# Performance work log

Hardware: AMD Instinct MI355X
Metric: run time of the kernel (lower is better)

The kernel has to match this reference:

```python
import jax, jax.numpy as jnp
import numpy as np
from jax import lax

C = 64
EPS = 1e-6

def ln2d(x, w, b):
    # channel-wise LN over HxW per (n, c)
    mean = x.mean(axis=(2, 3), keepdims=True)
    var = ((x - mean) ** 2).mean(axis=(2, 3), keepdims=True)
    return (x - mean) / jnp.sqrt(var + EPS) * w + b

def pw(x, w, b):
    # 1x1 conv: w [O, I], b [O]
    return jnp.einsum('nihw,oi->nohw', x, w) + b[None, :, None, None]

def dwconv3(x, w, b):
    # depthwise 3x3, w [2C, 1, 3, 3]
    y = lax.conv_general_dilated(x, w, window_strides=(1, 1), padding='SAME',
                                 feature_group_count=x.shape[1],
                                 dimension_numbers=('NCHW', 'OIHW', 'NCHW'))
    return y + b[None, :, None, None]

def simple_gate(x):
    x1, x2 = jnp.split(x, 2, axis=1)
    return x1 * x2

def setup_inputs() -> dict:
    key = jax.random.key(0)
    ks = jax.random.split(key, 16)
    s = 0.05
    return {
        'x': jax.random.normal(ks[0], (8, C, 256, 256), jnp.float32),
        'ln1_w': jnp.ones((1, C, 1, 1), jnp.float32),
        'ln1_b': jnp.zeros((1, C, 1, 1), jnp.float32),
        'pw1_w': jax.random.normal(ks[1], (2 * C, C), jnp.float32) * s,
        'pw1_b': jnp.zeros((2 * C,), jnp.float32),
        'dw_w': jax.random.normal(ks[2], (2 * C, 1, 3, 3), jnp.float32) * s,
        'dw_b': jnp.zeros((2 * C,), jnp.float32),
        'sca_w': jax.random.normal(ks[3], (C, C), jnp.float32) * s,
        'sca_b': jnp.zeros((C,), jnp.float32),
        'pw2_w': jax.random.normal(ks[4], (C, C), jnp.float32) * s,
        'pw2_b': jnp.zeros((C,), jnp.float32),
        'ln2_w': jnp.ones((1, C, 1, 1), jnp.float32),
        'ln2_b': jnp.zeros((1, C, 1, 1), jnp.float32),
        'pw3_w': jax.random.normal(ks[5], (2 * C, C), jnp.float32) * s,
        'pw3_b': jnp.zeros((2 * C,), jnp.float32),
        'pw4_w': jax.random.normal(ks[6], (C, C), jnp.float32) * s,
        'pw4_b': jnp.zeros((C,), jnp.float32),
        'beta1': jax.random.normal(ks[7], (1, C, 1, 1), jnp.float32) * 0.1,
        'beta2': jax.random.normal(ks[8], (1, C, 1, 1), jnp.float32) * 0.1,
    }

def reference(x, ln1_w, ln1_b, pw1_w, pw1_b, dw_w, dw_b, sca_w, sca_b,
              pw2_w, pw2_b, ln2_w, ln2_b, pw3_w, pw3_b, pw4_w, pw4_b,
              beta1, beta2):
    y = ln2d(x, ln1_w, ln1_b)
    y = pw(y, pw1_w, pw1_b)
    y = dwconv3(y, dw_w, dw_b)
    y = simple_gate(y)
    # SCA: global avg pool -> 1x1 conv -> sigmoid scale
    s = y.mean(axis=(2, 3), keepdims=True)          # [N, C, 1, 1]
    w = jax.nn.sigmoid(pw(s, sca_w, sca_b))
    y = y * w
    y = pw(y, pw2_w, pw2_b)
    x = x + beta1 * y
    y2 = ln2d(x, ln2_w, ln2_b)
    y2 = pw(y2, pw3_w, pw3_b)
    y2 = simple_gate(y2)
    y2 = pw(y2, pw4_w, pw4_b)
    return x + beta2 * y2
```

## Files before the change

### kernel.cpp

```cpp
#include <hip/hip_runtime.h>
#include <hip/hip_bf16.h>

#define NB 8
#define HWP 65536

typedef __attribute__((ext_vector_type(8))) short short8;
typedef __attribute__((ext_vector_type(4))) float f32x4;

__device__ __forceinline__ short f2bf(float f) {
  union { float f; unsigned u; } v; v.f = f;
  return (short)((v.u + 0x7FFF + ((v.u >> 16) & 1)) >> 16);
}
__device__ __forceinline__ float bf2f(unsigned short u) {
  union { unsigned u; float f; } v; v.u = ((unsigned)u) << 16; return v.f;
}

__global__ __launch_bounds__(512) void ln_stats_kernel(
    const float* __restrict__ x, const float* __restrict__ lw,
    const float* __restrict__ lb, float* __restrict__ a, float* __restrict__ b) {
  int plane = blockIdx.x;
  int c = plane & 63;
  const float4* p4 = (const float4*)(x + (size_t)plane * HWP);
  float s = 0.f, s2 = 0.f;
  for (int i = threadIdx.x; i < HWP / 4; i += 512) {
    float4 v = p4[i];
    s  += v.x + v.y + v.z + v.w;
    s2 += v.x * v.x + v.y * v.y + v.z * v.z + v.w * v.w;
  }
  for (int off = 32; off; off >>= 1) {
    s  += __shfl_down(s, off);
    s2 += __shfl_down(s2, off);
  }
  __shared__ float ls[8], ls2[8];
  int wid = threadIdx.x >> 6, lid = threadIdx.x & 63;
  if (lid == 0) { ls[wid] = s; ls2[wid] = s2; }
  __syncthreads();
  if (threadIdx.x == 0) {
    float S = 0.f, S2 = 0.f;
    for (int k = 0; k < 8; k++) { S += ls[k]; S2 += ls2[k]; }
    float mean = S * (1.f / (float)HWP);
    float var  = S2 * (1.f / (float)HWP) - mean * mean;
    float rstd = rsqrtf(var + 1e-6f);
    float av = rstd * lw[c];
    a[plane] = av;
    b[plane] = lb[c] - mean * av;
  }
}

__global__ void fold_kernel(const float* __restrict__ w, const float* __restrict__ pb,
                            const float* __restrict__ a, const float* __restrict__ b,
                            unsigned short* __restrict__ wf16, float* __restrict__ cf, int O) {
  int idx = blockIdx.x * blockDim.x + threadIdx.x;
  if (idx >= NB * O) return;
  int n = idx / O, o = idx - n * O;
  int MT = O >> 4;
  const float* an = a + n * 64;
  const float* bn = b + n * 64;
  const float* wo = w + o * 64;
  int mt = o >> 4, cl = o & 15;
  float cc = pb[o];
  for (int i = 0; i < 64; i++) {
    float wv = wo[i];
    float wf = wv * an[i];
    cc += wv * bn[i];
    int ks = i >> 5, quad = (i >> 3) & 3, j = i & 7;
    wf16[((((size_t)(n * MT + mt) * 2 + ks) * 16 + cl) * 4 + quad) * 8 + j] =
        (unsigned short)f2bf(wf);
  }
  cf[idx] = cc;
}

__global__ __launch_bounds__(256, 2) void gemm_pw1_kernel(
    const float* __restrict__ x, const unsigned short* __restrict__ wf16,
    const float* __restrict__ cf, unsigned short* __restrict__ z) {
  int n = blockIdx.y;
  int lane = threadIdx.x & 63, wid = threadIdx.x >> 6;
  int col = lane & 15, quad = lane >> 4;
  const short8* wv8 = (const short8*)wf16 + (size_t)n * 1024;
  short8 a[8][2];
  #pragma unroll
  for (int mt = 0; mt < 8; mt++)
    #pragma unroll
    for (int ks = 0; ks < 2; ks++)
      a[mt][ks] = wv8[((mt * 2 + ks) * 16 + col) * 4 + quad];
  f32x4 cb[8];
  #pragma unroll
  for (int mt = 0; mt < 8; mt++)
    cb[mt] = *(const f32x4*)(cf + n * 128 + mt * 16 + quad * 4);
  const float* xn = x + (size_t)n * 64 * HWP;
  unsigned short* zn = z + (size_t)n * 128 * HWP;
  int pxbase = blockIdx.x * 128 + wid * 16 + col;

  auto load_b = [&](int p, short8* bf) {
    #pragma unroll
    for (int ks = 0; ks < 2; ks++) {
      short8 v;
      #pragma unroll
      for (int j = 0; j < 8; j++)
        v[j] = f2bf(xn[(size_t)(ks * 32 + quad * 8 + j) * HWP + p]);
      bf[ks] = v;
    }
  };

  short8 bb[2][2];
  load_b(pxbase, bb[0]);
  #pragma unroll
  for (int tile = 0; tile < 2; tile++) {
    int cur = tile & 1, nxt = cur ^ 1;
    int p = pxbase + tile * 64;
    if (tile < 1) load_b(p + 64, bb[nxt]);
    f32x4 acc[8];
    #pragma unroll
    for (int mt = 0; mt < 8; mt++) {
      acc[mt] = cb[mt];
      acc[mt] = __builtin_amdgcn_mfma_f32_16x16x32_bf16(a[mt][0], bb[cur][0], acc[mt], 0, 0, 0);
      acc[mt] = __builtin_amdgcn_mfma_f32_16x16x32_bf16(a[mt][1], bb[cur][1], acc[mt], 0, 0, 0);
    }
    #pragma unroll
    for (int mt = 0; mt < 8; mt++)
      #pragma unroll
      for (int r = 0; r < 4; r++)
        zn[(size_t)(mt * 16 + quad * 4 + r) * HWP + p] =
            (unsigned short)f2bf(acc[mt][r]);
  }
}

__global__ __launch_bounds__(256) void dwgate_kernel(
    const unsigned short* __restrict__ z, const float* __restrict__ dww,
    const float* __restrict__ dwb, unsigned short* __restrict__ t,
    float* __restrict__ pooled4) {
  int blk = blockIdx.x;
  int plane = blk >> 2, qtr = blk & 3;
  int n = plane >> 6, c = plane & 63;
  int lane = threadIdx.x & 63, wv = threadIdx.x >> 6;
  const unsigned short* z0 = z + ((size_t)n * 128 + c) * HWP;
  const unsigned short* z1 = z0 + (size_t)64 * HWP;
  unsigned short* tp = t + (size_t)plane * HWP;
  float w0[9], w1[9];
  #pragma unroll
  for (int k = 0; k < 9; k++) { w0[k] = dww[c * 9 + k]; w1[k] = dww[(c + 64) * 9 + k]; }
  float bias0 = dwb[c], bias1 = dwb[c + 64];
  int r0 = qtr * 64 + wv * 16;
  int colb = lane * 4;

  float fa[3][4], la[3], ra[3];
  float fb[3][4], lb_[3], rb[3];

  auto loadrow = [&](const unsigned short* base, int h, float* f, float& l, float& r) {
    if ((unsigned)h < 256u) {
      ushort4 u = *(const ushort4*)(base + h * 256 + colb);
      f[0] = bf2f(u.x); f[1] = bf2f(u.y); f[2] = bf2f(u.z); f[3] = bf2f(u.w);
    } else {
      f[0] = f[1] = f[2] = f[3] = 0.f;
    }
    float ll = __shfl_up(f[3], 1);
    float rr = __shfl_down(f[0], 1);
    l = (lane == 0) ? 0.f : ll;
    r = (lane == 63) ? 0.f : rr;
  };

  loadrow(z0, r0 - 1, fa[0], la[0], ra[0]);
  loadrow(z1, r0 - 1, fb[0], lb_[0], rb[0]);
  loadrow(z0, r0,     fa[1], la[1], ra[1]);
  loadrow(z1, r0,     fb[1], lb_[1], rb[1]);

  float lsum = 0.f;
  #pragma unroll 2
  for (int h = r0; h < r0 + 16; h++) {
    loadrow(z0, h + 1, fa[2], la[2], ra[2]);
    loadrow(z1, h + 1, fb[2], lb_[2], rb[2]);
    float o0[4] = {bias0, bias0, bias0, bias0};
    float o1[4] = {bias1, bias1, bias1, bias1};
    #pragma unroll
    for (int rr_ = 0; rr_ < 3; rr_++) {
      float wl0 = w0[rr_ * 3], wc0 = w0[rr_ * 3 + 1], wr0 = w0[rr_ * 3 + 2];
      float wl1 = w1[rr_ * 3], wc1 = w1[rr_ * 3 + 1], wr1 = w1[rr_ * 3 + 2];
      const float* f0 = fa[rr_]; const float* f1 = fb[rr_];
      float l0 = la[rr_], r0h = ra[rr_], l1 = lb_[rr_], r1h = rb[rr_];
      o0[0] += wl0 * l0    + wc0 * f0[0] + wr0 * f0[1];
      o0[1] += wl0 * f0[0] + wc0 * f0[1] + wr0 * f0[2];
      o0[2] += wl0 * f0[1] + wc0 * f0[2] + wr0 * f0[3];
      o0[3] += wl0 * f0[2] + wc0 * f0[3] + wr0 * r0h;
      o1[0] += wl1 * l1    + wc1 * f1[0] + wr1 * f1[1];
      o1[1] += wl1 * f1[0] + wc1 * f1[1] + wr1 * f1[2];
      o1[2] += wl1 * f1[1] + wc1 * f1[2] + wr1 * f1[3];
      o1[3] += wl1 * f1[2] + wc1 * f1[3] + wr1 * r1h;
    }
    float g0 = o0[0] * o1[0], g1 = o0[1] * o1[1];
    float g2 = o0[2] * o1[2], g3 = o0[3] * o1[3];
    uint2 pk;
    pk.x = (unsigned)(unsigned short)f2bf(g0) | ((unsigned)(unsigned short)f2bf(g1) << 16);
    pk.y = (unsigned)(unsigned short)f2bf(g2) | ((unsigned)(unsigned short)f2bf(g3) << 16);
    *(uint2*)(tp + (size_t)h * 256 + colb) = pk;
    lsum += (g0 + g1) + (g2 + g3);
    #pragma unroll
    for (int i = 0; i < 4; i++) { fa[0][i] = fa[1][i]; fa[1][i] = fa[2][i];
                                  fb[0][i] = fb[1][i]; fb[1][i] = fb[2][i]; }
    la[0] = la[1]; la[1] = la[2]; ra[0] = ra[1]; ra[1] = ra[2];
    lb_[0] = lb_[1]; lb_[1] = lb_[2]; rb[0] = rb[1]; rb[1] = rb[2];
  }
  for (int off = 32; off; off >>= 1) lsum += __shfl_down(lsum, off);
  __shared__ float ls[4];
  if (lane == 0) ls[wv] = lsum;
  __syncthreads();
  if (threadIdx.x == 0) pooled4[plane * 4 + qtr] = ls[0] + ls[1] + ls[2] + ls[3];
}

__global__ void sca_kernel(const float* __restrict__ pooled4, const float* __restrict__ sw,
                           const float* __restrict__ sb, float* __restrict__ sca) {
  int idx = blockIdx.x * blockDim.x + threadIdx.x;
  if (idx >= 512) return;
  int n = idx >> 6, o = idx & 63;
  float s = sb[o];
  const float* pm = pooled4 + n * 256;
  for (int i = 0; i < 64; i++)
    s += sw[o * 64 + i] * (pm[i * 4] + pm[i * 4 + 1] + pm[i * 4 + 2] + pm[i * 4 + 3]) *
         (1.f / 65536.f);
  sca[idx] = 1.f / (1.f + expf(-s));
}

__global__ void fold_pw2_kernel(const float* __restrict__ w, const float* __restrict__ pb,
                                const float* __restrict__ sca, const float* __restrict__ beta1,
                                unsigned short* __restrict__ wf16, float* __restrict__ cf) {
  int idx = blockIdx.x * blockDim.x + threadIdx.x;
  if (idx >= 512) return;
  int n = idx >> 6, o = idx & 63;
  float bt = beta1[o];
  const float* sn = sca + n * 64;
  int mt = o >> 4, cl = o & 15;
  for (int i = 0; i < 64; i++) {
    float wf = bt * w[o * 64 + i] * sn[i];
    int ks = i >> 5, quad = (i >> 3) & 3, j = i & 7;
    wf16[((((size_t)(n * 4 + mt) * 2 + ks) * 16 + cl) * 4 + quad) * 8 + j] =
        (unsigned short)f2bf(wf);
  }
  cf[idx] = bt * pb[o];
}

__global__ void fold4_kernel(const float* __restrict__ w4, const float* __restrict__ pb4,
                             const float* __restrict__ beta2,
                             unsigned short* __restrict__ wf16, float* __restrict__ cf) {
  int o = threadIdx.x;
  if (o >= 64) return;
  float bt = beta2[o];
  int mt = o >> 4, cl = o & 15;
  for (int i = 0; i < 64; i++) {
    int ks = i >> 5, quad = (i >> 3) & 3, j = i & 7;
    wf16[((((size_t)mt * 2 + ks) * 16 + cl) * 4 + quad) * 8 + j] =
        (unsigned short)f2bf(bt * w4[o * 64 + i]);
  }
  cf[o] = bt * pb4[o];
}

__global__ __launch_bounds__(256, 2) void gemm_pw2_kernel(
    const unsigned short* __restrict__ t, const float* __restrict__ x,
    const unsigned short* __restrict__ wf16, const float* __restrict__ cf,
    float* __restrict__ x1, float* __restrict__ part_sum, float* __restrict__ part_sq) {
  __shared__ float red_s[4][64], red_q[4][64];
  int n = blockIdx.y;
  int lane = threadIdx.x & 63, wid = threadIdx.x >> 6;
  int col = lane & 15, quad = lane >> 4;
  const short8* wv8 = (const short8*)wf16 + (size_t)n * 512;
  short8 a[4][2];
  #pragma unroll
  for (int mt = 0; mt < 4; mt++)
    #pragma unroll
    for (int ks = 0; ks < 2; ks++)
      a[mt][ks] = wv8[((mt * 2 + ks) * 16 + col) * 4 + quad];
  f32x4 cb[4];
  #pragma unroll
  for (int mt = 0; mt < 4; mt++)
    cb[mt] = *(const f32x4*)(cf + n * 64 + mt * 16 + quad * 4);
  const unsigned short* tn = t + (size_t)n * 64 * HWP;
  const float* xn = x + (size_t)n * 64 * HWP;
  float* x1n = x1 + (size_t)n * 64 * HWP;
  int pxbase = blockIdx.x * 128 + wid * 16 + col;

  auto load_t = [&](int p, short8* bf) {
    #pragma unroll
    for (int ks = 0; ks < 2; ks++) {
      short8 v;
      #pragma unroll
      for (int j = 0; j < 8; j++)
        v[j] = (short)tn[(size_t)(ks * 32 + quad * 8 + j) * HWP + p];
      bf[ks] = v;
    }
  };
  auto load_x = [&](int p, float (*xv)[4]) {
    #pragma unroll
    for (int mt = 0; mt < 4; mt++)
      #pragma unroll
      for (int r = 0; r < 4; r++)
        xv[mt][r] = xn[(size_t)(mt * 16 + quad * 4 + r) * HWP + p];
  };

  float sacc[4][4], qacc[4][4];
  #pragma unroll
  for (int mt = 0; mt < 4; mt++)
    #pragma unroll
    for (int r = 0; r < 4; r++) { sacc[mt][r] = 0.f; qacc[mt][r] = 0.f; }

  short8 bb[2][2];
  float xv[2][4][4];
  load_t(pxbase, bb[0]);
  load_x(pxbase, xv[0]);
  #pragma unroll
  for (int tile = 0; tile < 2; tile++) {
    int cur = tile & 1, nxt = cur ^ 1;
    int p = pxbase + tile * 64;
    if (tile < 1) { load_t(p + 64, bb[nxt]); load_x(p + 64, xv[nxt]); }
    f32x4 acc[4];
    #pragma unroll
    for (int mt = 0; mt < 4; mt++) {
      acc[mt] = cb[mt];
      acc[mt] = __builtin_amdgcn_mfma_f32_16x16x32_bf16(a[mt][0], bb[cur][0], acc[mt], 0, 0, 0);
      acc[mt] = __builtin_amdgcn_mfma_f32_16x16x32_bf16(a[mt][1], bb[cur][1], acc[mt], 0, 0, 0);
    }
    #pragma unroll
    for (int mt = 0; mt < 4; mt++)
      #pragma unroll
      for (int r = 0; r < 4; r++) {
        size_t idx = (size_t)(mt * 16 + quad * 4 + r) * HWP + p;
        float v = xv[cur][mt][r] + acc[mt][r];
        x1n[idx] = v;
        sacc[mt][r] += v;
        qacc[mt][r] += v * v;
      }
  }
  #pragma unroll
  for (int mt = 0; mt < 4; mt++)
    #pragma unroll
    for (int r = 0; r < 4; r++) {
      float s = sacc[mt][r], q = qacc[mt][r];
      #pragma unroll
      for (int off = 1; off < 16; off <<= 1) {
        s += __shfl_xor(s, off);
        q += __shfl_xor(q, off);
      }
      if (col == 0) {
        int o = mt * 16 + quad * 4 + r;
        red_s[wid][o] = s; red_q[wid][o] = q;
      }
    }
  __syncthreads();
  if (threadIdx.x < 64) {
    int c = threadIdx.x;
    float s = red_s[0][c] + red_s[1][c] + red_s[2][c] + red_s[3][c];
    float q = red_q[0][c] + red_q[1][c] + red_q[2][c] + red_q[3][c];
    size_t pidx = ((size_t)n * 64 + c) * 512 + blockIdx.x;
    part_sum[pidx] = s;
    part_sq[pidx]  = q;
  }
}

__global__ __launch_bounds__(256) void ln2fold_kernel(
    const float* __restrict__ w, const float* __restrict__ pb,
    const float* __restrict__ ps, const float* __restrict__ pq,
    const float* __restrict__ lw, const float* __restrict__ lb,
    unsigned short* __restrict__ wf16, float* __restrict__ cf) {
  __shared__ float aa[64], bbv[64];
  int n = blockIdx.x;
  if (threadIdx.x < 64) {
    int c = threadIdx.x;
    const float* p1 = ps + ((size_t)n * 64 + c) * 512;
    const float* p2 = pq + ((size_t)n * 64 + c) * 512;
    float S = 0.f, S2 = 0.f;
    for (int k = 0; k < 512; k++) { S += p1[k]; S2 += p2[k]; }
    float mean = S * (1.f / (float)HWP);
    float var  = S2 * (1.f / (float)HWP) - mean * mean;
    float rstd = rsqrtf(var + 1e-6f);
    float av = rstd * lw[c];
    aa[c] = av;
    bbv[c] = lb[c] - mean * av;
  }
  __syncthreads();
  if (threadIdx.x < 128) {
    int o = threadIdx.x;
    const float* wo = w + o * 64;
    int mt = o >> 4, cl = o & 15;
    float cc = pb[o];
    for (int i = 0; i < 64; i++) {
      float wv = wo[i];
      float wf = wv * aa[i];
      cc += wv * bbv[i];
      int ks = i >> 5, quad = (i >> 3) & 3, j = i & 7;
      wf16[((((size_t)(n * 8 + mt) * 2 + ks) * 16 + cl) * 4 + quad) * 8 + j] =
          (unsigned short)f2bf(wf);
    }
    cf[n * 128 + o] = cc;
  }
}

__global__ __launch_bounds__(256, 2) void final_mfma_kernel(
    const float* __restrict__ x1, const unsigned short* __restrict__ w3f16,
    const float* __restrict__ c3f, const unsigned short* __restrict__ w4f16,
    const float* __restrict__ c4f, float* __restrict__ out) {
  __shared__ float s_c3[128];
  __shared__ __align__(16) float s_c4[64];
  int n = blockIdx.y;
  int lane = threadIdx.x & 63, wid = threadIdx.x >> 6;
  int col = lane & 15, quad = lane >> 4;
  if (threadIdx.x < 128) s_c3[threadIdx.x] = c3f[n * 128 + threadIdx.x];
  if (threadIdx.x < 64) s_c4[threadIdx.x] = c4f[threadIdx.x];
  const short8* w3v = (const short8*)w3f16 + (size_t)n * 1024;
  short8 a3[8][2];
  #pragma unroll
  for (int mt = 0; mt < 8; mt++)
    #pragma unroll
    for (int ks = 0; ks < 2; ks++)
      a3[mt][ks] = w3v[((mt * 2 + ks) * 16 + col) * 4 + quad];
  const short8* w4v = (const short8*)w4f16;
  short8 a4[4][2];
  #pragma unroll
  for (int mt = 0; mt < 4; mt++)
    #pragma unroll
    for (int ks = 0; ks < 2; ks++)
      a4[mt][ks] = w4v[((mt * 2 + ks) * 16 + col) * 4 + quad];
  __syncthreads();
  const float* x1n = x1 + (size_t)n * 64 * HWP;
  float* outn = out + (size_t)n * 64 * HWP;
  int pxbase = blockIdx.x * 128 + wid * 16 + col;

  auto load_b1 = [&](int p, short8* bf) {
    #pragma unroll
    for (int ks = 0; ks < 2; ks++) {
      short8 v;
      #pragma unroll
      for (int j = 0; j < 8; j++)
        v[j] = f2bf(x1n[(size_t)(ks * 32 + quad * 8 + j) * HWP + p]);
      bf[ks] = v;
    }
  };

  short8 bb1[2][2];
  load_b1(pxbase, bb1[0]);
  #pragma unroll
  for (int tile = 0; tile < 2; tile++) {
    int cur = tile & 1, nxt = cur ^ 1;
    int p = pxbase + tile * 64;
    if (tile < 1) load_b1(p + 64, bb1[nxt]);
    f32x4 acc[8];
    #pragma unroll
    for (int mt = 0; mt < 8; mt++) {
      acc[mt] = (f32x4){0.f, 0.f, 0.f, 0.f};
      acc[mt] = __builtin_amdgcn_mfma_f32_16x16x32_bf16(a3[mt][0], bb1[cur][0], acc[mt], 0, 0, 0);
      acc[mt] = __builtin_amdgcn_mfma_f32_16x16x32_bf16(a3[mt][1], bb1[cur][1], acc[mt], 0, 0, 0);
    }
    unsigned pd[4][2];
    #pragma unroll
    for (int mt = 0; mt < 4; mt++)
      #pragma unroll
      for (int u = 0; u < 2; u++) {
        int c0 = mt * 16 + quad * 4 + 2 * u;
        float ga = (acc[mt][2 * u]     + s_c3[c0])     * (acc[mt + 4][2 * u]     + s_c3[64 + c0]);
        float gb = (acc[mt][2 * u + 1] + s_c3[c0 + 1]) * (acc[mt + 4][2 * u + 1] + s_c3[64 + c0 + 1]);
        pd[mt][u] = (unsigned)(unsigned short)f2bf(ga) |
                    ((unsigned)(unsigned short)f2bf(gb) << 16);
      }
    short8 b2f[2];
    #pragma unroll
    for (int ks = 0; ks < 2; ks++)
      #pragma unroll
      for (int w = 0; w < 4; w++) {
        int src = ((quad & 1) * 2 + (w >> 1)) * 16 + col;
        unsigned v0 = (unsigned)__shfl((int)pd[ks * 2][w & 1], src, 64);
        unsigned v1 = (unsigned)__shfl((int)pd[ks * 2 + 1][w & 1], src, 64);
        unsigned u = (quad & 2) ? v1 : v0;
        b2f[ks][2 * w]     = (short)(u & 0xFFFFu);
        b2f[ks][2 * w + 1] = (short)(u >> 16);
      }
    f32x4 acc2[4];
    #pragma unroll
    for (int mt = 0; mt < 4; mt++) {
      acc2[mt] = *(const f32x4*)&s_c4[mt * 16 + quad * 4];
      acc2[mt] = __builtin_amdgcn_mfma_f32_16x16x32_bf16(a4[mt][0], b2f[0], acc2[mt], 0, 0, 0);
      acc2[mt] = __builtin_amdgcn_mfma_f32_16x16x32_bf16(a4[mt][1], b2f[1], acc2[mt], 0, 0, 0);
    }
    #pragma unroll
    for (int mt = 0; mt < 4; mt++)
      #pragma unroll
      for (int r = 0; r < 4; r++) {
        size_t idx = (size_t)(mt * 16 + quad * 4 + r) * HWP + p;
        outn[idx] = x1n[idx] + acc2[mt][r];
      }
  }
}

extern "C" void kernel_launch(void* const* d_in, const int* in_sizes, int n_in,
                              void* d_out, int out_size, void* d_ws, size_t ws_size,
                              hipStream_t stream) {
  const float* x    = (const float*)d_in[0];
  const float* ln1w = (const float*)d_in[1];
  const float* ln1b = (const float*)d_in[2];
  const float* pw1w = (const float*)d_in[3];
  const float* pw1b = (const float*)d_in[4];
  const float* dww  = (const float*)d_in[5];
  const float* dwb  = (const float*)d_in[6];
  const float* scaw = (const float*)d_in[7];
  const float* scab = (const float*)d_in[8];
  const float* pw2w = (const float*)d_in[9];
  const float* pw2b = (const float*)d_in[10];
  const float* ln2w = (const float*)d_in[11];
  const float* ln2b = (const float*)d_in[12];
  const float* pw3w = (const float*)d_in[13];
  const float* pw3b = (const float*)d_in[14];
  const float* pw4w = (const float*)d_in[15];
  const float* pw4b = (const float*)d_in[16];
  const float* beta1= (const float*)d_in[17];
  const float* beta2= (const float*)d_in[18];
  float* out = (float*)d_out;

  char* ws = (char*)d_ws;
  unsigned short* z  = (unsigned short*)ws;
  float*          x1 = (float*)ws;
  unsigned short* t  = (unsigned short*)(ws + 134217728ull);
  float* sm = (float*)(ws + 134217728ull + 67108864ull);
  float* a1 = sm;
  float* b1 = a1 + 512;
  float* c1f = b1 + 512;
  float* pooled4 = c1f + 1024;
  float* sca = pooled4 + 2048;
  float* c2f = sca + 512;
  float* c3f = c2f + 512;
  float* c4f = c3f + 1024;
  unsigned short* w1f16 = (unsigned short*)(c4f + 64);
  unsigned short* w2f16 = w1f16 + 65536;
  unsigned short* w3f16 = w2f16 + 32768;
  unsigned short* w4f16 = w3f16 + 65536;
  float* part_sum = (float*)d_out;
  float* part_sq  = part_sum + 262144;

  hipLaunchKernelGGL(ln_stats_kernel, dim3(512), dim3(512), 0, stream, x, ln1w, ln1b, a1, b1);
  hipLaunchKernelGGL(fold_kernel, dim3(4), dim3(256), 0, stream, pw1w, pw1b, a1, b1, w1f16, c1f, 128);
  hipLaunchKernelGGL(fold4_kernel, dim3(1), dim3(64), 0, stream, pw4w, pw4b, beta2, w4f16, c4f);
  hipLaunchKernelGGL(gemm_pw1_kernel, dim3(512, 8), dim3(256), 0, stream, x, w1f16, c1f, z);
  hipLaunchKernelGGL(dwgate_kernel, dim3(2048), dim3(256), 0, stream, z, dww, dwb, t, pooled4);
  hipLaunchKernelGGL(sca_kernel, dim3(2), dim3(256), 0, stream, pooled4, scaw, scab, sca);
  hipLaunchKernelGGL(fold_pw2_kernel, dim3(2), dim3(256), 0, stream, pw2w, pw2b, sca, beta1, w2f16, c2f);
  hipLaunchKernelGGL(gemm_pw2_kernel, dim3(512, 8), dim3(256), 0, stream, t, x, w2f16, c2f, x1,
                     part_sum, part_sq);
  hipLaunchKernelGGL(ln2fold_kernel, dim3(8), dim3(256), 0, stream,
                     pw3w, pw3b, part_sum, part_sq, ln2w, ln2b, w3f16, c3f);
  hipLaunchKernelGGL(final_mfma_kernel, dim3(512, 8), dim3(256), 0, stream,
                     x1, w3f16, c3f, w4f16, c4f, out);
}
```

Measured before the change: 563.6 us.

## Pad intermediate plane strides, fuse SCA with pw2 fold, parallelize LN2 reduction

Intermediate buffers z, t and x1 now use padded per-channel strides instead of an exact power of two. This is meant to cut cache and channel conflicts when the GEMM kernels access 64-128 channel planes at the same pixel offset. The SCA and pw2 weight-fold kernels are merged into one launch that passes the sigmoid scales through shared memory. The LN2 statistics reduction now uses four threads per channel with shuffle reduction instead of one serial thread. Workspace offsets grow slightly to fit the padding.

```diff
diff --git a/kernel.cpp b/kernel.cpp
--- a/kernel.cpp
+++ b/kernel.cpp
@@ -3,6 +3,9 @@
 
 #define NB 8
 #define HWP 65536
+#define ZS  65664
+#define TS  65664
+#define XS  65600
 
 typedef __attribute__((ext_vector_type(8))) short short8;
 typedef __attribute__((ext_vector_type(4))) float f32x4;
@@ -70,6 +73,21 @@
   cf[idx] = cc;
 }
 
+__global__ void fold4_kernel(const float* __restrict__ w4, const float* __restrict__ pb4,
+                             const float* __restrict__ beta2,
+                             unsigned short* __restrict__ wf16, float* __restrict__ cf) {
+  int o = threadIdx.x;
+  if (o >= 64) return;
+  float bt = beta2[o];
+  int mt = o >> 4, cl = o & 15;
+  for (int i = 0; i < 64; i++) {
+    int ks = i >> 5, quad = (i >> 3) & 3, j = i & 7;
+    wf16[((((size_t)mt * 2 + ks) * 16 + cl) * 4 + quad) * 8 + j] =
+        (unsigned short)f2bf(bt * w4[o * 64 + i]);
+  }
+  cf[o] = bt * pb4[o];
+}
+
 __global__ __launch_bounds__(256, 2) void gemm_pw1_kernel(
     const float* __restrict__ x, const unsigned short* __restrict__ wf16,
     const float* __restrict__ cf, unsigned short* __restrict__ z) {
@@ -88,7 +106,7 @@
   for (int mt = 0; mt < 8; mt++)
     cb[mt] = *(const f32x4*)(cf + n * 128 + mt * 16 + quad * 4);
   const float* xn = x + (size_t)n * 64 * HWP;
-  unsigned short* zn = z + (size_t)n * 128 * HWP;
+  unsigned short* zn = z + (size_t)n * 128 * ZS;
   int pxbase = blockIdx.x * 128 + wid * 16 + col;
 
   auto load_b = [&](int p, short8* bf) {
@@ -120,7 +138,7 @@
     for (int mt = 0; mt < 8; mt++)
       #pragma unroll
       for (int r = 0; r < 4; r++)
-        zn[(size_t)(mt * 16 + quad * 4 + r) * HWP + p] =
+        zn[(size_t)(mt * 16 + quad * 4 + r) * ZS + p] =
             (unsigned short)f2bf(acc[mt][r]);
   }
 }
@@ -133,9 +151,9 @@
   int plane = blk >> 2, qtr = blk & 3;
   int n = plane >> 6, c = plane & 63;
   int lane = threadIdx.x & 63, wv = threadIdx.x >> 6;
-  const unsigned short* z0 = z + ((size_t)n * 128 + c) * HWP;
-  const unsigned short* z1 = z0 + (size_t)64 * HWP;
-  unsigned short* tp = t + (size_t)plane * HWP;
+  const unsigned short* z0 = z + ((size_t)n * 128 + c) * ZS;
+  const unsigned short* z1 = z0 + (size_t)64 * ZS;
+  unsigned short* tp = t + (size_t)plane * TS;
   float w0[9], w1[9];
   #pragma unroll
   for (int k = 0; k < 9; k++) { w0[k] = dww[c * 9 + k]; w1[k] = dww[(c + 64) * 9 + k]; }
@@ -206,50 +224,30 @@
   if (threadIdx.x == 0) pooled4[plane * 4 + qtr] = ls[0] + ls[1] + ls[2] + ls[3];
 }
 
-__global__ void sca_kernel(const float* __restrict__ pooled4, const float* __restrict__ sw,
-                           const float* __restrict__ sb, float* __restrict__ sca) {
-  int idx = blockIdx.x * blockDim.x + threadIdx.x;
-  if (idx >= 512) return;
-  int n = idx >> 6, o = idx & 63;
+__global__ __launch_bounds__(256) void sca_fold_kernel(
+    const float* __restrict__ pooled4, const float* __restrict__ sw,
+    const float* __restrict__ sb, const float* __restrict__ w2,
+    const float* __restrict__ pb2, const float* __restrict__ beta1,
+    unsigned short* __restrict__ wf16, float* __restrict__ cf) {
+  __shared__ float scal[4][64];
+  int ln = threadIdx.x >> 6, o = threadIdx.x & 63;
+  int n = blockIdx.x * 4 + ln;
+  const float* pm = pooled4 + n * 256;
   float s = sb[o];
-  const float* pm = pooled4 + n * 256;
   for (int i = 0; i < 64; i++)
     s += sw[o * 64 + i] * (pm[i * 4] + pm[i * 4 + 1] + pm[i * 4 + 2] + pm[i * 4 + 3]) *
          (1.f / 65536.f);
-  sca[idx] = 1.f / (1.f + expf(-s));
-}
-
-__global__ void fold_pw2_kernel(const float* __restrict__ w, const float* __restrict__ pb,
-                                const float* __restrict__ sca, const float* __restrict__ beta1,
-                                unsigned short* __restrict__ wf16, float* __restrict__ cf) {
-  int idx = blockIdx.x * blockDim.x + threadIdx.x;
-  if (idx >= 512) return;
-  int n = idx >> 6, o = idx & 63;
+  scal[ln][o] = 1.f / (1.f + expf(-s));
+  __syncthreads();
   float bt = beta1[o];
-  const float* sn = sca + n * 64;
   int mt = o >> 4, cl = o & 15;
   for (int i = 0; i < 64; i++) {
-    float wf = bt * w[o * 64 + i] * sn[i];
+    float wf = bt * w2[o * 64 + i] * scal[ln][i];
     int ks = i >> 5, quad = (i >> 3) & 3, j = i & 7;
     wf16[((((size_t)(n * 4 + mt) * 2 + ks) * 16 + cl) * 4 + quad) * 8 + j] =
         (unsigned short)f2bf(wf);
   }
-  cf[idx] = bt * pb[o];
-}
-
-__global__ void fold4_kernel(const float* __restrict__ w4, const float* __restrict__ pb4,
-                             const float* __restrict__ beta2,
-                             unsigned short* __restrict__ wf16, float* __restrict__ cf) {
-  int o = threadIdx.x;
-  if (o >= 64) return;
-  float bt = beta2[o];
-  int mt = o >> 4, cl = o & 15;
-  for (int i = 0; i < 64; i++) {
-    int ks = i >> 5, quad = (i >> 3) & 3, j = i & 7;
-    wf16[((((size_t)mt * 2 + ks) * 16 + cl) * 4 + quad) * 8 + j] =
-        (unsigned short)f2bf(bt * w4[o * 64 + i]);
-  }
-  cf[o] = bt * pb4[o];
+  cf[n * 64 + o] = bt * pb2[o];
 }
 
 __global__ __launch_bounds__(256, 2) void gemm_pw2_kernel(
@@ -271,9 +269,9 @@
   #pragma unroll
   for (int mt = 0; mt < 4; mt++)
     cb[mt] = *(const f32x4*)(cf + n * 64 + mt * 16 + quad * 4);
-  const unsigned short* tn = t + (size_t)n * 64 * HWP;
+  const unsigned short* tn = t + (size_t)n * 64 * TS;
   const float* xn = x + (size_t)n * 64 * HWP;
-  float* x1n = x1 + (size_t)n * 64 * HWP;
+  float* x1n = x1 + (size_t)n * 64 * XS;
   int pxbase = blockIdx.x * 128 + wid * 16 + col;
 
   auto load_t = [&](int p, short8* bf) {
@@ -282,7 +280,7 @@
       short8 v;
       #pragma unroll
       for (int j = 0; j < 8; j++)
-        v[j] = (short)tn[(size_t)(ks * 32 + quad * 8 + j) * HWP + p];
+        v[j] = (short)tn[(size_t)(ks * 32 + quad * 8 + j) * TS + p];
       bf[ks] = v;
     }
   };
@@ -320,7 +318,7 @@
     for (int mt = 0; mt < 4; mt++)
       #pragma unroll
       for (int r = 0; r < 4; r++) {
-        size_t idx = (size_t)(mt * 16 + quad * 4 + r) * HWP + p;
+        size_t idx = (size_t)(mt * 16 + quad * 4 + r) * XS + p;
         float v = xv[cur][mt][r] + acc[mt][r];
         x1n[idx] = v;
         sacc[mt][r] += v;
@@ -360,12 +358,14 @@
     unsigned short* __restrict__ wf16, float* __restrict__ cf) {
   __shared__ float aa[64], bbv[64];
   int n = blockIdx.x;
-  if (threadIdx.x < 64) {
-    int c = threadIdx.x;
-    const float* p1 = ps + ((size_t)n * 64 + c) * 512;
-    const float* p2 = pq + ((size_t)n * 64 + c) * 512;
-    float S = 0.f, S2 = 0.f;
-    for (int k = 0; k < 512; k++) { S += p1[k]; S2 += p2[k]; }
+  int c = threadIdx.x >> 2, k4 = threadIdx.x & 3;
+  const float* p1 = ps + ((size_t)n * 64 + c) * 512 + k4 * 128;
+  const float* p2 = pq + ((size_t)n * 64 + c) * 512 + k4 * 128;
+  float S = 0.f, S2 = 0.f;
+  for (int k = 0; k < 128; k++) { S += p1[k]; S2 += p2[k]; }
+  S  += __shfl_xor(S, 1);  S  += __shfl_xor(S, 2);
+  S2 += __shfl_xor(S2, 1); S2 += __shfl_xor(S2, 2);
+  if (k4 == 0) {
     float mean = S * (1.f / (float)HWP);
     float var  = S2 * (1.f / (float)HWP) - mean * mean;
     float rstd = rsqrtf(var + 1e-6f);
@@ -417,7 +417,7 @@
     for (int ks = 0; ks < 2; ks++)
       a4[mt][ks] = w4v[((mt * 2 + ks) * 16 + col) * 4 + quad];
   __syncthreads();
-  const float* x1n = x1 + (size_t)n * 64 * HWP;
+  const float* x1n = x1 + (size_t)n * 64 * XS;
   float* outn = out + (size_t)n * 64 * HWP;
   int pxbase = blockIdx.x * 128 + wid * 16 + col;
 
@@ -427,7 +427,7 @@
       short8 v;
       #pragma unroll
       for (int j = 0; j < 8; j++)
-        v[j] = f2bf(x1n[(size_t)(ks * 32 + quad * 8 + j) * HWP + p]);
+        v[j] = f2bf(x1n[(size_t)(ks * 32 + quad * 8 + j) * XS + p]);
       bf[ks] = v;
     }
   };
@@ -480,8 +480,8 @@
     for (int mt = 0; mt < 4; mt++)
       #pragma unroll
       for (int r = 0; r < 4; r++) {
-        size_t idx = (size_t)(mt * 16 + quad * 4 + r) * HWP + p;
-        outn[idx] = x1n[idx] + acc2[mt][r];
+        size_t idx = (size_t)(mt * 16 + quad * 4 + r) * XS + p;
+        outn[(size_t)(mt * 16 + quad * 4 + r) * HWP + p] = x1n[idx] + acc2[mt][r];
       }
   }
 }
@@ -513,14 +513,13 @@
   char* ws = (char*)d_ws;
   unsigned short* z  = (unsigned short*)ws;
   float*          x1 = (float*)ws;
-  unsigned short* t  = (unsigned short*)(ws + 134217728ull);
-  float* sm = (float*)(ws + 134217728ull + 67108864ull);
+  unsigned short* t  = (unsigned short*)(ws + 134479872ull);
+  float* sm = (float*)(ws + 134479872ull + 67239936ull);
   float* a1 = sm;
   float* b1 = a1 + 512;
   float* c1f = b1 + 512;
   float* pooled4 = c1f + 1024;
-  float* sca = pooled4 + 2048;
-  float* c2f = sca + 512;
+  float* c2f = pooled4 + 2048;
   float* c3f = c2f + 512;
   float* c4f = c3f + 1024;
   unsigned short* w1f16 = (unsigned short*)(c4f + 64);
@@ -535,8 +534,8 @@
   hipLaunchKernelGGL(fold4_kernel, dim3(1), dim3(64), 0, stream, pw4w, pw4b, beta2, w4f16, c4f);
   hipLaunchKernelGGL(gemm_pw1_kernel, dim3(512, 8), dim3(256), 0, stream, x, w1f16, c1f, z);
   hipLaunchKernelGGL(dwgate_kernel, dim3(2048), dim3(256), 0, stream, z, dww, dwb, t, pooled4);
-  hipLaunchKernelGGL(sca_kernel, dim3(2), dim3(256), 0, stream, pooled4, scaw, scab, sca);
-  hipLaunchKernelGGL(fold_pw2_kernel, dim3(2), dim3(256), 0, stream, pw2w, pw2b, sca, beta1, w2f16, c2f);
+  hipLaunchKernelGGL(sca_fold_kernel, dim3(2), dim3(256), 0, stream,
+                     pooled4, scaw, scab, pw2w, pw2b, beta1, w2f16, c2f);
   hipLaunchKernelGGL(gemm_pw2_kernel, dim3(512, 8), dim3(256), 0, stream, t, x, w2f16, c2f, x1,
                      part_sum, part_sq);
   hipLaunchKernelGGL(ln2fold_kernel, dim3(8), dim3(256), 0, stream,
```

Measured after the change: 562.2 us. About the same (-0.3%).
